# Performance work log

Hardware: AMD Instinct MI355X
Metric: run time of the kernel (lower is better)

## Reference

```python
import jax, jax.numpy as jnp
import numpy as np

NUM_GRAPHS = 64
LEAKY_SLOPE = 0.2
LN_EPS = 1e-5


def setup_inputs() -> dict:
    key = jax.random.key(0)
    ks = jax.random.split(key, 32)
    N, E = 100000, 1600000
    H, C, D = 4, 32, 128
    L = 4
    inp = {}
    inp['x'] = jax.random.normal(ks[0], (N, 8), dtype=jnp.float32)
    inp['edge_index'] = jax.random.randint(ks[1], (2, E), 0, N, dtype=jnp.int64)
    inp['edge_attr'] = jax.random.normal(ks[2], (E, 3), dtype=jnp.float32)
    inp['batch'] = jnp.sort(jax.random.randint(ks[3], (N,), 0, NUM_GRAPHS, dtype=jnp.int64))
    s = 0.05
    inp['node_w'] = jax.random.normal(ks[4], (8, D), dtype=jnp.float32) * s
    inp['node_b'] = jax.random.normal(ks[5], (D,), dtype=jnp.float32) * s
    inp['edge_w'] = jax.random.normal(ks[6], (3, D), dtype=jnp.float32) * s
    inp['edge_b'] = jax.random.normal(ks[7], (D,), dtype=jnp.float32) * s
    inp['gat_lin'] = jax.random.normal(ks[8], (L, D, D), dtype=jnp.float32) * s
    inp['gat_att_src'] = jax.random.normal(ks[9], (L, H, C), dtype=jnp.float32) * s
    inp['gat_att_dst'] = jax.random.normal(ks[10], (L, H, C), dtype=jnp.float32) * s
    inp['gat_lin_edge'] = jax.random.normal(ks[11], (L, D, D), dtype=jnp.float32) * s
    inp['gat_att_edge'] = jax.random.normal(ks[12], (L, H, C), dtype=jnp.float32) * s
    inp['gat_bias'] = jax.random.normal(ks[13], (L, D), dtype=jnp.float32) * s
    inp['ln_g'] = jnp.ones((L, D), dtype=jnp.float32)
    inp['ln_b'] = jnp.zeros((L, D), dtype=jnp.float32)
    inp['dos_w1'] = jax.random.normal(ks[14], (D, D // 2), dtype=jnp.float32) * s
    inp['dos_b1'] = jax.random.normal(ks[15], (D // 2,), dtype=jnp.float32) * s
    inp['dos_w2'] = jax.random.normal(ks[16], (D // 2, 100), dtype=jnp.float32) * s
    inp['dos_b2'] = jax.random.normal(ks[17], (100,), dtype=jnp.float32) * s
    inp['trans_w1'] = jax.random.normal(ks[18], (D, D // 2), dtype=jnp.float32) * s
    inp['trans_b1'] = jax.random.normal(ks[19], (D // 2,), dtype=jnp.float32) * s
    inp['trans_w2'] = jax.random.normal(ks[20], (D // 2, 100), dtype=jnp.float32) * s
    inp['trans_b2'] = jax.random.normal(ks[21], (100,), dtype=jnp.float32) * s
    return inp


def _gat_layer(x, ea, src, dst, lin, a_s, a_d, lin_e, a_e, bias):
    # PyG GATConv (concat=True, add_self_loops=True, fill_value='mean'), eval mode.
    N = x.shape[0]
    H, C = a_s.shape
    h = (x @ lin).reshape(N, H, C)            # [N,H,C]
    # add self loops; self-loop edge_attr = mean of edge_attr over edges
    loop = jnp.arange(N, dtype=src.dtype)
    src_f = jnp.concatenate([src, loop])
    dst_f = jnp.concatenate([dst, loop])
    ea_mean = jnp.broadcast_to(ea.mean(axis=0), (N, ea.shape[1]))
    ea_f = jnp.concatenate([ea, ea_mean], axis=0)
    e = (ea_f @ lin_e).reshape(-1, H, C)      # [E+N,H,C]
    a_src = (h * a_s).sum(-1)                 # [N,H]
    a_dst = (h * a_d).sum(-1)                 # [N,H]
    alpha = a_src[src_f] + a_dst[dst_f] + (e * a_e).sum(-1)  # [E+N,H]
    alpha = jnp.where(alpha >= 0, alpha, LEAKY_SLOPE * alpha)
    # segment softmax over destination nodes
    m = jax.ops.segment_max(alpha, dst_f, num_segments=N)
    ex = jnp.exp(alpha - m[dst_f])
    denom = jax.ops.segment_sum(ex, dst_f, num_segments=N)
    w = ex / (denom[dst_f] + 1e-16)           # [E+N,H]
    msg = h[src_f] * w[:, :, None]            # [E+N,H,C]
    out = jax.ops.segment_sum(msg, dst_f, num_segments=N)
    return out.reshape(N, H * C) + bias


def _layer_norm(x, g, b):
    mu = x.mean(-1, keepdims=True)
    var = ((x - mu) ** 2).mean(-1, keepdims=True)
    return (x - mu) * jax.lax.rsqrt(var + LN_EPS) * g + b


def reference(x, edge_index, edge_attr, batch, node_w, node_b, edge_w, edge_b,
              gat_lin, gat_att_src, gat_att_dst, gat_lin_edge, gat_att_edge,
              gat_bias, ln_g, ln_b, dos_w1, dos_b1, dos_w2, dos_b2,
              trans_w1, trans_b1, trans_w2, trans_b2):
    src, dst = edge_index[0], edge_index[1]
    h = x @ node_w + node_b                   # [N,128]
    ea = edge_attr @ edge_w + edge_b          # [E,128]
    L = gat_lin.shape[0]
    for i in range(L):
        h = _gat_layer(h, ea, src, dst, gat_lin[i], gat_att_src[i],
                       gat_att_dst[i], gat_lin_edge[i], gat_att_edge[i], gat_bias[i])
        h = _layer_norm(h, ln_g[i], ln_b[i])
        h = jax.nn.relu(h)
        # dropout is identity in eval mode
    # global mean pool over graphs
    sums = jax.ops.segment_sum(h, batch, num_segments=NUM_GRAPHS)
    cnts = jax.ops.segment_sum(jnp.ones((h.shape[0], 1), h.dtype), batch, num_segments=NUM_GRAPHS)
    g = sums / jnp.maximum(cnts, 1.0)         # [G,128]
    dos = jax.nn.relu(g @ dos_w1 + dos_b1) @ dos_w2 + dos_b2
    trans = jax.nn.relu(g @ trans_w1 + trans_b1) @ trans_w2 + trans_b2
    return (dos, trans)
```

## Files before the change

kernel.cpp:

```cpp
#include <hip/hip_runtime.h>

#define LEAKY 0.2f
#define LN_EPSV 1e-5f
#define NGRAPH 64

typedef __attribute__((ext_vector_type(8))) short short8v;
typedef __attribute__((ext_vector_type(4))) float f32x4;

static __device__ __forceinline__ float leakyf(float x){ return x >= 0.f ? x : LEAKY*x; }

static __device__ __forceinline__ unsigned short f2bf(float f){
  unsigned int u = __float_as_uint(f);
  u = (u + 0x7fffu + ((u >> 16) & 1u)) >> 16;
  return (unsigned short)u;
}
static __device__ __forceinline__ float bf2f(unsigned short v){
  return __uint_as_float(((unsigned int)v) << 16);
}

__global__ void front_k(const float* __restrict__ x, const float* __restrict__ w,
                        const float* __restrict__ b, unsigned short* __restrict__ hb, int N,
                        const float* __restrict__ ea, float* __restrict__ emean,
                        const int* __restrict__ dst, int* __restrict__ cnt, int E){
  int stride = gridDim.x*blockDim.x;
  int tid0 = blockIdx.x*blockDim.x + threadIdx.x;
  for(int tid = tid0; tid < N*32; tid += stride){
    int n = tid >> 5; int c4 = (tid & 31) * 4;
    float xr[8];
    #pragma unroll
    for (int k=0;k<8;k++) xr[k] = x[(size_t)n*8+k];
    float4 acc = *(const float4*)&b[c4];
    #pragma unroll
    for (int k=0;k<8;k++){
      float4 wv = *(const float4*)&w[k*128 + c4];
      acc.x += xr[k]*wv.x; acc.y += xr[k]*wv.y; acc.z += xr[k]*wv.z; acc.w += xr[k]*wv.w;
    }
    ushort4 o; o.x=f2bf(acc.x); o.y=f2bf(acc.y); o.z=f2bf(acc.z); o.w=f2bf(acc.w);
    *(ushort4*)&hb[(size_t)n*128 + c4] = o;
  }
  float s0=0.f,s1=0.f,s2=0.f;
  for (int e = tid0; e < E; e += stride){
    s0 += ea[(size_t)e*3]; s1 += ea[(size_t)e*3+1]; s2 += ea[(size_t)e*3+2];
    atomicAdd(&cnt[dst[e]], 1);
  }
  #pragma unroll
  for (int m=32;m;m>>=1){ s0 += __shfl_xor(s0,m); s1 += __shfl_xor(s1,m); s2 += __shfl_xor(s2,m); }
  __shared__ float ls[3][8];
  int wv = threadIdx.x>>6;
  if ((threadIdx.x&63)==0){ ls[0][wv]=s0; ls[1][wv]=s1; ls[2][wv]=s2; }
  __syncthreads();
  if (threadIdx.x==0){
    float a=0.f,bb=0.f,c=0.f;
    int nw = blockDim.x>>6;
    for(int i=0;i<nw;i++){ a+=ls[0][i]; bb+=ls[1][i]; c+=ls[2][i]; }
    atomicAdd(&emean[0],a); atomicAdd(&emean[1],bb); atomicAdd(&emean[2],c);
  }
}

__global__ void scan1_k(const int* __restrict__ in, int* __restrict__ incl, int* __restrict__ bsum, int n){
  __shared__ int s[1024];
  int i = blockIdx.x*1024 + threadIdx.x;
  int v = (i<n)? in[i]:0;
  s[threadIdx.x]=v; __syncthreads();
  for(int off=1;off<1024;off<<=1){
    int t = (threadIdx.x>=off)? s[threadIdx.x-off] : 0;
    __syncthreads();
    s[threadIdx.x]+=t; __syncthreads();
  }
  if(i<n) incl[i]=s[threadIdx.x];
  if(threadIdx.x==1023) bsum[blockIdx.x]=s[1023];
}
__global__ void scan2_k(const int* __restrict__ bsum, int* __restrict__ boff, int nb){
  if(threadIdx.x==0 && blockIdx.x==0){
    int run=0;
    for(int i=0;i<nb;i++){ boff[i]=run; run+=bsum[i]; }
  }
}
__global__ void scan3_k(const int* __restrict__ incl, const int* __restrict__ boff, int* __restrict__ row_ptr, int n){
  int i = blockIdx.x*blockDim.x + threadIdx.x;
  if(i<n) row_ptr[i+1] = incl[i] + boff[i>>10];
  if(i==0) row_ptr[0]=0;
}

__global__ void csr_fill_k(const int* __restrict__ src, const int* __restrict__ dst,
                           const float* __restrict__ eattr,
                           const int* __restrict__ row_ptr, int* __restrict__ cnt,
                           float4* __restrict__ csr_rec, int E){
  int t = blockIdx.x*blockDim.x + threadIdx.x;
  int e0 = t*4;
  if (e0+3 < E){
    float4 a0 = *(const float4*)&eattr[(size_t)e0*3];
    float4 a1 = *(const float4*)&eattr[(size_t)e0*3+4];
    float4 a2 = *(const float4*)&eattr[(size_t)e0*3+8];
    int4 d4 = *(const int4*)&dst[e0];
    int4 s4 = *(const int4*)&src[e0];
    int p0 = row_ptr[d4.x] + atomicAdd(&cnt[d4.x],1);
    int p1 = row_ptr[d4.y] + atomicAdd(&cnt[d4.y],1);
    int p2 = row_ptr[d4.z] + atomicAdd(&cnt[d4.z],1);
    int p3 = row_ptr[d4.w] + atomicAdd(&cnt[d4.w],1);
    csr_rec[p0] = make_float4(a0.x,a0.y,a0.z, __int_as_float(s4.x));
    csr_rec[p1] = make_float4(a0.w,a1.x,a1.y, __int_as_float(s4.y));
    csr_rec[p2] = make_float4(a1.z,a1.w,a2.x, __int_as_float(s4.z));
    csr_rec[p3] = make_float4(a2.y,a2.z,a2.w, __int_as_float(s4.w));
  } else {
    for(int e=e0; e<E; ++e){
      int d = dst[e];
      int pos = row_ptr[d] + atomicAdd(&cnt[d],1);
      csr_rec[pos] = make_float4(eattr[(size_t)e*3], eattr[(size_t)e*3+1], eattr[(size_t)e*3+2],
                                 __int_as_float(src[e]));
    }
  }
}

__global__ void precompute_k(const float* __restrict__ lin_e, const float* __restrict__ a_e,
                             const float* __restrict__ edge_w, const float* __restrict__ edge_b,
                             const float* __restrict__ emean_sum, float invE,
                             float* __restrict__ params){
  int l = blockIdx.x; int t = threadIdx.x;
  __shared__ float Ve[128][4];
  __shared__ float sW3[12]; __shared__ float sce[4];
  const float* Le = lin_e + (size_t)l*16384; const float* Ae = a_e + l*128;
  #pragma unroll
  for(int h=0; h<4; h++){
    float v=0.f;
    for(int c=0;c<32;c++) v += Le[t*128 + h*32 + c]*Ae[h*32+c];
    Ve[t][h]=v;
  }
  __syncthreads();
  float* P = params + l*32;
  if(t<12){ int k=t>>2, h=t&3; float v=0.f; for(int d=0;d<128;d++) v += edge_w[k*128+d]*Ve[d][h]; P[t]=v; sW3[t]=v; }
  if(t>=16 && t<20){ int h=t-16; float v=0.f; for(int d=0;d<128;d++) v += edge_b[d]*Ve[d][h]; P[12+h]=v; sce[h]=v; }
  __syncthreads();
  if(t<4){
    float v = sce[t];
    for(int k=0;k<3;k++) v += emean_sum[k]*invE * sW3[k*4+t];
    P[16+t]=v;
  }
}

__global__ void prepack_w_k(const float* __restrict__ gat_lin, short8v* __restrict__ wpack){
  int l = blockIdx.x; int t = threadIdx.x;
  const float* W = gat_lin + (size_t)l*16384;
  for(int f = t; f < 2048; f += 256){
    int j = f >> 8, ks = (f >> 6) & 3, lane = f & 63;
    int lo = lane & 15, hi = (lane >> 4) & 3;
    short8v b;
    #pragma unroll
    for(int e=0;e<8;e++) b[e] = (short)f2bf(W[(size_t)(ks*32 + hi*8 + e)*128 + j*16 + lo]);
    wpack[(size_t)l*2048 + f] = b;
  }
}

__global__ __launch_bounds__(256) void mfma_dense_k(const unsigned short* __restrict__ hin,
    const short8v* __restrict__ wpack, const float* __restrict__ att_s, const float* __restrict__ att_d,
    unsigned short* __restrict__ hbf, float* __restrict__ a_src, float* __restrict__ a_dst,
    int N, int ntiles){
  int lane = threadIdx.x & 63;
  int wid  = threadIdx.x >> 6;
  int lo = lane & 15, hi = lane >> 4;
  short8v Bf[8][4];
  #pragma unroll
  for(int j=0;j<8;j++){
    #pragma unroll
    for(int ks=0;ks<4;ks++)
      Bf[j][ks] = wpack[(j<<8) + (ks<<6) + lane];
  }
  float as[8], ad[8];
  #pragma unroll
  for(int j=0;j<8;j++){ as[j]=att_s[j*16+lo]; ad[j]=att_d[j*16+lo]; }

  for(int t = blockIdx.x*4 + wid; t < ntiles; t += gridDim.x*4){
    int n0 = t*16;
    int arow = n0 + lo; if(arow >= N) arow = N-1;
    short8v A[4];
    #pragma unroll
    for(int ks=0;ks<4;ks++)
      A[ks] = *(const short8v*)&hin[(size_t)arow*128 + ks*32 + hi*8];
    float ps[4][4], pd[4][4];
    #pragma unroll
    for(int r=0;r<4;r++){
      #pragma unroll
      for(int h=0;h<4;h++){ ps[r][h]=0.f; pd[r][h]=0.f; }
    }
    #pragma unroll
    for(int j=0;j<8;j++){
      f32x4 acc = {0.f,0.f,0.f,0.f};
      #pragma unroll
      for(int ks=0;ks<4;ks++)
        acc = __builtin_amdgcn_mfma_f32_16x16x32_bf16(A[ks], Bf[j][ks], acc, 0, 0, 0);
      int h = j>>1;
      #pragma unroll
      for(int r=0;r<4;r++){
        int row = n0 + hi*4 + r;
        if(row < N) hbf[(size_t)row*128 + j*16 + lo] = f2bf(acc[r]);
        ps[r][h] += acc[r]*as[j];
        pd[r][h] += acc[r]*ad[j];
      }
    }
    #pragma unroll
    for(int r=0;r<4;r++){
      #pragma unroll
      for(int h=0;h<4;h++){
        #pragma unroll
        for(int msk=1; msk<16; msk<<=1){
          ps[r][h] += __shfl_xor(ps[r][h], msk);
          pd[r][h] += __shfl_xor(pd[r][h], msk);
        }
      }
    }
    if(lo==0){
      #pragma unroll
      for(int r=0;r<4;r++){
        int row = n0 + hi*4 + r;
        if(row<N){
          *(float4*)&a_src[(size_t)row*4] = make_float4(ps[r][0],ps[r][1],ps[r][2],ps[r][3]);
          *(float4*)&a_dst[(size_t)row*4] = make_float4(pd[r][0],pd[r][1],pd[r][2],pd[r][3]);
        }
      }
    }
  }
}

__global__ void aggregate_k(const unsigned int* __restrict__ hbf, const float* __restrict__ a_src,
    const float* __restrict__ a_dst, const int* __restrict__ row_ptr,
    const float4* __restrict__ csr_rec, const float* __restrict__ params,
    const float* __restrict__ bias, const float* __restrict__ lng, const float* __restrict__ lnb,
    unsigned int* __restrict__ h_out, int N){
  int lane = threadIdx.x & 63;
  int n = blockIdx.x*(blockDim.x>>6) + (threadIdx.x>>6);
  if(n>=N) return;
  int g  = lane >> 4;
  int eh = lane & 3;
  int ee = lane >> 2;
  float W0 = params[eh], W1 = params[4+eh], W2 = params[8+eh];
  float ce = params[12+eh], aes = params[16+eh];
  float adst = a_dst[n*4+eh];
  float m = leakyf(a_src[n*4+eh] + adst + aes);
  float dpart = (ee==0) ? 1.f : 0.f;
  float2 acc;
  {
    unsigned int u = hbf[(size_t)n*64 + lane];
    acc.x = __uint_as_float(u << 16);
    acc.y = __uint_as_float(u & 0xffff0000u);
  }
  int s = row_ptr[n], e = row_ptr[n+1];
  for(int base=s; base<e; base+=16){
    int nv = e - base; if(nv>16) nv=16;
    int sr = 0; float al = -1e30f;
    if(ee < nv){
      float4 rc = csr_rec[base+ee];
      sr = __float_as_int(rc.w);
      al = leakyf(a_src[sr*4+eh] + adst + rc.x*W0 + rc.y*W1 + rc.z*W2 + ce);
    }
    float cm = al;
    cm = fmaxf(cm, __shfl_xor(cm,4));
    cm = fmaxf(cm, __shfl_xor(cm,8));
    cm = fmaxf(cm, __shfl_xor(cm,16));
    cm = fmaxf(cm, __shfl_xor(cm,32));
    float nm = fmaxf(m, cm);
    float sc = __expf(m - nm);
    float p  = __expf(al - nm);
    dpart = dpart*sc + p;
    m = nm;
    unsigned int u[16];
    #pragma unroll
    for(int q=0;q<16;q++){
      int srq = __shfl(sr, q*4);
      u[q] = hbf[(size_t)srq*64 + lane];
    }
    float scg = __shfl(sc, g);
    acc.x *= scg; acc.y *= scg;
    #pragma unroll
    for(int q=0;q<16;q++){
      float pq = __shfl(p, q*4 + g);
      float hx = __uint_as_float(u[q] << 16);
      float hy = __uint_as_float(u[q] & 0xffff0000u);
      acc.x += pq*hx; acc.y += pq*hy;
    }
  }
  float dsum = dpart;
  dsum += __shfl_xor(dsum,4);
  dsum += __shfl_xor(dsum,8);
  dsum += __shfl_xor(dsum,16);
  dsum += __shfl_xor(dsum,32);
  float inv = 1.f/(__shfl(dsum, g) + 1e-16f);
  int c = lane*2;
  float ox = acc.x*inv + bias[c], oy = acc.y*inv + bias[c+1];
  float sum = ox+oy;
  #pragma unroll
  for(int msk=32;msk;msk>>=1) sum += __shfl_xor(sum,msk);
  float mean = sum*(1.f/128.f);
  float dx = ox-mean, dy = oy-mean;
  float sq = dx*dx + dy*dy;
  #pragma unroll
  for(int msk=32;msk;msk>>=1) sq += __shfl_xor(sq,msk);
  float r = rsqrtf(sq*(1.f/128.f) + LN_EPSV);
  float yx = fmaxf(dx*r*lng[c]  + lnb[c],   0.f);
  float yy = fmaxf(dy*r*lng[c+1]+ lnb[c+1], 0.f);
  h_out[(size_t)n*64 + lane] = (unsigned int)f2bf(yx) | ((unsigned int)f2bf(yy) << 16);
}

__global__ void pool_k(const unsigned short* __restrict__ h, const int* __restrict__ batch,
                       float* __restrict__ sums, float* __restrict__ cntf, int N){
  int t = threadIdx.x;
  int n0 = blockIdx.x*256;
  int nend = n0+256; if (nend > N) nend = N;
  float acc = 0.f; float runc = 0.f; int curb = -1;
  for(int n=n0;n<nend;n++){
    int b = batch[n];
    if(b!=curb){
      if(curb>=0){ atomicAdd(&sums[curb*128+t], acc); if(t==0) atomicAdd(&cntf[curb], runc); }
      acc=0.f; runc=0.f; curb=b;
    }
    acc += bf2f(h[(size_t)n*128+t]);
    runc += 1.f;
  }
  if(curb>=0){ atomicAdd(&sums[curb*128+t], acc); if(t==0) atomicAdd(&cntf[curb], runc); }
}

__global__ void heads_k(const float* __restrict__ sums, const float* __restrict__ cntf,
    const float* __restrict__ w1a, const float* __restrict__ b1a,
    const float* __restrict__ w2a, const float* __restrict__ b2a,
    const float* __restrict__ w1b, const float* __restrict__ b1b,
    const float* __restrict__ w2b, const float* __restrict__ b2b,
    float* __restrict__ out){
  int g = blockIdx.x, t = threadIdx.x;
  __shared__ float gv[128]; __shared__ float hid[64];
  float c = fmaxf(cntf[g], 1.f);
  gv[t] = sums[g*128+t] / c;
  __syncthreads();
  if(t<64){ float v=b1a[t]; for(int d=0;d<128;d++) v += gv[d]*w1a[d*64+t]; hid[t]=fmaxf(v,0.f); }
  __syncthreads();
  if(t<100){ float v=b2a[t]; for(int j=0;j<64;j++) v += hid[j]*w2a[j*100+t]; out[g*100+t]=v; }
  __syncthreads();
  if(t<64){ float v=b1b[t]; for(int d=0;d<128;d++) v += gv[d]*w1b[d*64+t]; hid[t]=fmaxf(v,0.f); }
  __syncthreads();
  if(t<100){ float v=b2b[t]; for(int j=0;j<64;j++) v += hid[j]*w2b[j*100+t]; out[6400 + g*100+t]=v; }
}

extern "C" void kernel_launch(void* const* d_in, const int* in_sizes, int n_in,
                              void* d_out, int out_size, void* d_ws, size_t ws_size,
                              hipStream_t stream){
  const float* x      = (const float*)d_in[0];
  const int*   ei     = (const int*)d_in[1];
  const float* eattr  = (const float*)d_in[2];
  const int*   batch  = (const int*)d_in[3];
  const float* node_w = (const float*)d_in[4];
  const float* node_b = (const float*)d_in[5];
  const float* edge_w = (const float*)d_in[6];
  const float* edge_b = (const float*)d_in[7];
  const float* gat_lin= (const float*)d_in[8];
  const float* att_s  = (const float*)d_in[9];
  const float* att_d  = (const float*)d_in[10];
  const float* lin_e  = (const float*)d_in[11];
  const float* att_e  = (const float*)d_in[12];
  const float* gat_bias=(const float*)d_in[13];
  const float* ln_g   = (const float*)d_in[14];
  const float* ln_b   = (const float*)d_in[15];

  const int N = in_sizes[0]/8;
  const int E = in_sizes[2]/3;
  const int* srcp = ei;
  const int* dstp = ei + E;

  char* wp = (char*)d_ws;
  auto alloc = [&](size_t bytes)->char*{ char* p = wp; wp += (bytes+255)&~(size_t)255; return p; };
  unsigned short* hb_node  = (unsigned short*) alloc((size_t)N*128*2);
  unsigned short* hbf_tab  = (unsigned short*) alloc((size_t)N*128*2);
  float*  a_srcb  = (float*) alloc((size_t)N*4*4);
  float*  a_dstb  = (float*) alloc((size_t)N*4*4);
  int*    row_ptr = (int*)   alloc((size_t)(N+1)*4);
  int*    cnt     = (int*)   alloc((size_t)N*4);
  float4* csr_rec = (float4*)alloc((size_t)E*16);
  int*    incl    = (int*)   alloc((size_t)N*4);
  int     nb      = (N+1023)/1024;
  int*    bsum    = (int*)   alloc((size_t)nb*4);
  int*    boff    = (int*)   alloc((size_t)nb*4);
  float*  emean   = (float*) alloc(16);
  float*  params  = (float*) alloc(4*32*4);
  float*  psums   = (float*) alloc(64*128*4);
  float*  pcnt    = (float*) alloc(64*4);
  short8v* wpack  = (short8v*)alloc((size_t)4*2048*16);
  (void)ws_size; (void)n_in; (void)out_size;

  hipMemsetAsync(cnt, 0, (size_t)N*4, stream);
  hipMemsetAsync(emean, 0, 16, stream);
  hipMemsetAsync(psums, 0, 64*128*4, stream);
  hipMemsetAsync(pcnt, 0, 64*4, stream);

  front_k<<<2048, 256, 0, stream>>>(x, node_w, node_b, hb_node, N, eattr, emean, dstp, cnt, E);
  scan1_k<<<nb, 1024, 0, stream>>>(cnt, incl, bsum, N);
  scan2_k<<<1, 64, 0, stream>>>(bsum, boff, nb);
  scan3_k<<<(N+255)/256, 256, 0, stream>>>(incl, boff, row_ptr, N);
  hipMemsetAsync(cnt, 0, (size_t)N*4, stream);
  csr_fill_k<<<((E+3)/4+255)/256, 256, 0, stream>>>(srcp, dstp, eattr, row_ptr, cnt, csr_rec, E);
  precompute_k<<<4, 128, 0, stream>>>(lin_e, att_e, edge_w, edge_b, emean, 1.0f/(float)E, params);
  prepack_w_k<<<4, 256, 0, stream>>>(gat_lin, wpack);

  int ntiles = (N+15)/16;
  for(int l=0;l<4;l++){
    mfma_dense_k<<<1024, 256, 0, stream>>>(hb_node, wpack + (size_t)l*2048,
        att_s + l*128, att_d + l*128, hbf_tab, a_srcb, a_dstb, N, ntiles);
    aggregate_k<<<(N+3)/4, 256, 0, stream>>>((const unsigned int*)hbf_tab, a_srcb, a_dstb,
        row_ptr, csr_rec,
        params + l*32, gat_bias + l*128, ln_g + l*128, ln_b + l*128,
        (unsigned int*)hb_node, N);
  }

  pool_k<<<(N+255)/256, 128, 0, stream>>>(hb_node, batch, psums, pcnt, N);
  heads_k<<<64, 128, 0, stream>>>(psums, pcnt,
      (const float*)d_in[16], (const float*)d_in[17], (const float*)d_in[18], (const float*)d_in[19],
      (const float*)d_in[20], (const float*)d_in[21], (const float*)d_in[22], (const float*)d_in[23],
      (float*)d_out);
}
```

Before: 808.0 us.

## Shard CSR degree counters into eight shadow copies to cut atomic contention

```diff
diff --git a/kernel.cpp b/kernel.cpp
--- a/kernel.cpp
+++ b/kernel.cpp
@@ -21,7 +21,7 @@
 __global__ void front_k(const float* __restrict__ x, const float* __restrict__ w,
                         const float* __restrict__ b, unsigned short* __restrict__ hb, int N,
                         const float* __restrict__ ea, float* __restrict__ emean,
-                        const int* __restrict__ dst, int* __restrict__ cnt, int E){
+                        const int* __restrict__ dst, int* __restrict__ cnt8, int E){
   int stride = gridDim.x*blockDim.x;
   int tid0 = blockIdx.x*blockDim.x + threadIdx.x;
   for(int tid = tid0; tid < N*32; tid += stride){
@@ -39,9 +39,28 @@
     *(ushort4*)&hb[(size_t)n*128 + c4] = o;
   }
   float s0=0.f,s1=0.f,s2=0.f;
-  for (int e = tid0; e < E; e += stride){
-    s0 += ea[(size_t)e*3]; s1 += ea[(size_t)e*3+1]; s2 += ea[(size_t)e*3+2];
-    atomicAdd(&cnt[dst[e]], 1);
+  int nt4 = (E+3)>>2;
+  for (int t4 = tid0; t4 < nt4; t4 += stride){
+    int e0 = t4*4;
+    int bsh = (t4 & 7) * N;
+    if (e0+3 < E){
+      float4 a0 = *(const float4*)&ea[(size_t)e0*3];
+      float4 a1 = *(const float4*)&ea[(size_t)e0*3+4];
+      float4 a2 = *(const float4*)&ea[(size_t)e0*3+8];
+      int4 d4 = *(const int4*)&dst[e0];
+      s0 += a0.x + a0.w + a1.z + a2.y;
+      s1 += a0.y + a1.x + a1.w + a2.z;
+      s2 += a0.z + a1.y + a2.x + a2.w;
+      atomicAdd(&cnt8[bsh + d4.x], 1);
+      atomicAdd(&cnt8[bsh + d4.y], 1);
+      atomicAdd(&cnt8[bsh + d4.z], 1);
+      atomicAdd(&cnt8[bsh + d4.w], 1);
+    } else {
+      for(int e=e0; e<E; ++e){
+        s0 += ea[(size_t)e*3]; s1 += ea[(size_t)e*3+1]; s2 += ea[(size_t)e*3+2];
+        atomicAdd(&cnt8[bsh + dst[e]], 1);
+      }
+    }
   }
   #pragma unroll
   for (int m=32;m;m>>=1){ s0 += __shfl_xor(s0,m); s1 += __shfl_xor(s1,m); s2 += __shfl_xor(s2,m); }
@@ -57,10 +76,14 @@
   }
 }
 
-__global__ void scan1_k(const int* __restrict__ in, int* __restrict__ incl, int* __restrict__ bsum, int n){
+__global__ void scan1_k(const int* __restrict__ cnt8, int* __restrict__ incl, int* __restrict__ bsum, int n){
   __shared__ int s[1024];
   int i = blockIdx.x*1024 + threadIdx.x;
-  int v = (i<n)? in[i]:0;
+  int v = 0;
+  if(i<n){
+    #pragma unroll
+    for(int bsh=0;bsh<8;bsh++) v += cnt8[bsh*n + i];
+  }
   s[threadIdx.x]=v; __syncthreads();
   for(int off=1;off<1024;off<<=1){
     int t = (threadIdx.x>=off)? s[threadIdx.x-off] : 0;
@@ -82,22 +105,35 @@
   if(i==0) row_ptr[0]=0;
 }
 
+__global__ void shadowbase_k(const int* __restrict__ row_ptr, int* __restrict__ cnt8, int n){
+  int i = blockIdx.x*blockDim.x + threadIdx.x;
+  if(i>=n) return;
+  int run = row_ptr[i];
+  #pragma unroll
+  for(int bsh=0;bsh<8;bsh++){
+    int tmp = cnt8[bsh*n + i];
+    cnt8[bsh*n + i] = run;
+    run += tmp;
+  }
+}
+
 __global__ void csr_fill_k(const int* __restrict__ src, const int* __restrict__ dst,
                            const float* __restrict__ eattr,
-                           const int* __restrict__ row_ptr, int* __restrict__ cnt,
-                           float4* __restrict__ csr_rec, int E){
+                           int* __restrict__ cnt8,
+                           float4* __restrict__ csr_rec, int N, int E){
   int t = blockIdx.x*blockDim.x + threadIdx.x;
   int e0 = t*4;
+  int bsh = (t & 7) * N;
   if (e0+3 < E){
     float4 a0 = *(const float4*)&eattr[(size_t)e0*3];
     float4 a1 = *(const float4*)&eattr[(size_t)e0*3+4];
     float4 a2 = *(const float4*)&eattr[(size_t)e0*3+8];
     int4 d4 = *(const int4*)&dst[e0];
     int4 s4 = *(const int4*)&src[e0];
-    int p0 = row_ptr[d4.x] + atomicAdd(&cnt[d4.x],1);
-    int p1 = row_ptr[d4.y] + atomicAdd(&cnt[d4.y],1);
-    int p2 = row_ptr[d4.z] + atomicAdd(&cnt[d4.z],1);
-    int p3 = row_ptr[d4.w] + atomicAdd(&cnt[d4.w],1);
+    int p0 = atomicAdd(&cnt8[bsh + d4.x],1);
+    int p1 = atomicAdd(&cnt8[bsh + d4.y],1);
+    int p2 = atomicAdd(&cnt8[bsh + d4.z],1);
+    int p3 = atomicAdd(&cnt8[bsh + d4.w],1);
     csr_rec[p0] = make_float4(a0.x,a0.y,a0.z, __int_as_float(s4.x));
     csr_rec[p1] = make_float4(a0.w,a1.x,a1.y, __int_as_float(s4.y));
     csr_rec[p2] = make_float4(a1.z,a1.w,a2.x, __int_as_float(s4.z));
@@ -105,7 +141,7 @@
   } else {
     for(int e=e0; e<E; ++e){
       int d = dst[e];
-      int pos = row_ptr[d] + atomicAdd(&cnt[d],1);
+      int pos = atomicAdd(&cnt8[bsh + d],1);
       csr_rec[pos] = make_float4(eattr[(size_t)e*3], eattr[(size_t)e*3+1], eattr[(size_t)e*3+2],
                                  __int_as_float(src[e]));
     }
@@ -370,7 +406,7 @@
   float*  a_srcb  = (float*) alloc((size_t)N*4*4);
   float*  a_dstb  = (float*) alloc((size_t)N*4*4);
   int*    row_ptr = (int*)   alloc((size_t)(N+1)*4);
-  int*    cnt     = (int*)   alloc((size_t)N*4);
+  int*    cnt8    = (int*)   alloc((size_t)8*N*4);
   float4* csr_rec = (float4*)alloc((size_t)E*16);
   int*    incl    = (int*)   alloc((size_t)N*4);
   int     nb      = (N+1023)/1024;
@@ -383,17 +419,17 @@
   short8v* wpack  = (short8v*)alloc((size_t)4*2048*16);
   (void)ws_size; (void)n_in; (void)out_size;
 
-  hipMemsetAsync(cnt, 0, (size_t)N*4, stream);
+  hipMemsetAsync(cnt8, 0, (size_t)8*N*4, stream);
   hipMemsetAsync(emean, 0, 16, stream);
   hipMemsetAsync(psums, 0, 64*128*4, stream);
   hipMemsetAsync(pcnt, 0, 64*4, stream);
 
-  front_k<<<2048, 256, 0, stream>>>(x, node_w, node_b, hb_node, N, eattr, emean, dstp, cnt, E);
-  scan1_k<<<nb, 1024, 0, stream>>>(cnt, incl, bsum, N);
+  front_k<<<2048, 256, 0, stream>>>(x, node_w, node_b, hb_node, N, eattr, emean, dstp, cnt8, E);
+  scan1_k<<<nb, 1024, 0, stream>>>(cnt8, incl, bsum, N);
   scan2_k<<<1, 64, 0, stream>>>(bsum, boff, nb);
   scan3_k<<<(N+255)/256, 256, 0, stream>>>(incl, boff, row_ptr, N);
-  hipMemsetAsync(cnt, 0, (size_t)N*4, stream);
-  csr_fill_k<<<((E+3)/4+255)/256, 256, 0, stream>>>(srcp, dstp, eattr, row_ptr, cnt, csr_rec, E);
+  shadowbase_k<<<(N+255)/256, 256, 0, stream>>>(row_ptr, cnt8, N);
+  csr_fill_k<<<((E+3)/4+255)/256, 256, 0, stream>>>(srcp, dstp, eattr, cnt8, csr_rec, N, E);
   precompute_k<<<4, 128, 0, stream>>>(lin_e, att_e, edge_w, edge_b, emean, 1.0f/(float)E, params);
   prepack_w_k<<<4, 256, 0, stream>>>(gat_lin, wpack);
 
```

Result: slower. 826.4 us (+2.3%).
